# Optimization experiments

Hardware: AMD Instinct MI355X
Metric: run time of the kernel (lower is better)

Reference implementation:

```python
import jax, jax.numpy as jnp
import numpy as np

VOL = (256, 256, 256)
K = 64  # number of connected components (clusters)


def setup_inputs() -> dict:
    key = jax.random.key(0)
    k1, k2, k3 = jax.random.split(key, 3)
    # Precomputed connected-component labels of (pred + target) > 0.
    # 0 = background, 1..K = clusters.
    labels = jax.random.randint(k1, VOL, 0, K + 1, dtype=jnp.int32)
    fg = labels > 0
    # Binary prediction / ground-truth masks, nonzero only inside labeled regions
    # (consistent with labels being components of the overlay of pred and target).
    pred = ((jax.random.uniform(k2, VOL) < 0.6) & fg).astype(jnp.float32)
    target = ((jax.random.uniform(k3, VOL) < 0.6) & fg).astype(jnp.float32)
    return {"pred": pred, "target": target, "labels": labels, "num_clusters": K}


def reference(pred, target, labels, num_clusters):
    # Per-cluster dice via one fused segment reduction instead of a Python loop
    # over clusters. Segment 0 is background and is dropped, matching
    # range(1, num_features + 1) in the original.
    lab = labels.reshape(-1)
    p = pred.reshape(-1)
    t = target.reshape(-1)
    nseg = num_clusters + 1
    # intersection = sum(pred_cluster * gt_cluster); pred/target are binary so
    # logical_and(...).float() products reduce to pred * target per segment.
    inter = jax.ops.segment_sum(p * t, lab, num_segments=nseg)[1:]
    sum_p = jax.ops.segment_sum(p, lab, num_segments=nseg)[1:]
    sum_t = jax.ops.segment_sum(t, lab, num_segments=nseg)[1:]
    union = sum_p + sum_t
    dice = jnp.where(union > 0, 2.0 * inter / jnp.maximum(union, 1.0), 1.0)
    return 1.0 - jnp.mean(dice)
```

## Files before the change

kernel.cpp:

```cpp
#include <hip/hip_runtime.h>


#define NBIN 65
#define NREP 64
#define REP_MASK 63
#define BLOCKS 1024
#define THREADS 256

__device__ __forceinline__ unsigned short contrib16(float p, float t) {
    unsigned int sp = (p != 0.0f) ? 1u : 0u;
    unsigned int st = (t != 0.0f) ? 1u : 0u;
    return (unsigned short)(((sp & st) << 8) | (sp + st));
}

__device__ __forceinline__ void rmw4(unsigned short* col, float4 p, float4 t, int4 l) {
    col[l.x * THREADS] = (unsigned short)(col[l.x * THREADS] + contrib16(p.x, t.x));
    col[l.y * THREADS] = (unsigned short)(col[l.y * THREADS] + contrib16(p.y, t.y));
    col[l.z * THREADS] = (unsigned short)(col[l.z * THREADS] + contrib16(p.z, t.z));
    col[l.w * THREADS] = (unsigned short)(col[l.w * THREADS] + contrib16(p.w, t.w));
}

__global__ __launch_bounds__(THREADS, 4) void seg_count_kernel(
    const float* __restrict__ pred,
    const float* __restrict__ target,
    const int* __restrict__ labels,
    unsigned long long* __restrict__ part,
    int n)
{
    __shared__ unsigned short s_hist[NBIN][THREADS];
    const int tid = threadIdx.x;
    const int rep = (int)blockIdx.x & REP_MASK;

    unsigned int* hz = (unsigned int*)s_hist;
    for (int i = tid; i < NBIN * THREADS / 2; i += THREADS) hz[i] = 0u;
    __syncthreads();

    const int n_vec = n >> 2;
    const float4* __restrict__ p4 = (const float4*)pred;
    const float4* __restrict__ t4 = (const float4*)target;
    const int4*   __restrict__ l4 = (const int4*)labels;

    const int chunk = (n_vec + (int)gridDim.x - 1) / (int)gridDim.x;
    const int base = blockIdx.x * chunk;
    const int end = min(base + chunk, n_vec);

    unsigned short* col = &s_hist[0][tid];

    int idx = base + tid;
    for (; idx + 3 * THREADS < end; idx += 4 * THREADS) {
        float4 p0 = p4[idx];
        float4 p1 = p4[idx + THREADS];
        float4 p2 = p4[idx + 2 * THREADS];
        float4 p3 = p4[idx + 3 * THREADS];
        float4 t0 = t4[idx];
        float4 t1 = t4[idx + THREADS];
        float4 t2 = t4[idx + 2 * THREADS];
        float4 t3 = t4[idx + 3 * THREADS];
        int4   l0 = l4[idx];
        int4   l1 = l4[idx + THREADS];
        int4   l2 = l4[idx + 2 * THREADS];
        int4   l3 = l4[idx + 3 * THREADS];
        __builtin_amdgcn_sched_barrier(0);
        rmw4(col, p0, t0, l0);
        rmw4(col, p1, t1, l1);
        rmw4(col, p2, t2, l2);
        rmw4(col, p3, t3, l3);
    }
    for (; idx < end; idx += THREADS)
        rmw4(col, p4[idx], t4[idx], l4[idx]);

    if (blockIdx.x == 0) {
        for (int i = (n_vec << 2) + tid; i < n; i += THREADS)
            col[labels[i] * THREADS] =
                (unsigned short)(col[labels[i] * THREADS] + contrib16(pred[i], target[i]));
    }
    __syncthreads();

    const int s = 1 + (tid >> 2);
    const int q = tid & 3;
    const unsigned long long* row = (const unsigned long long*)&s_hist[s][q * 64];
    unsigned long long accU = 0, accI = 0;
    const int rot = tid & 15;
    #pragma unroll
    for (int j = 0; j < 16; ++j) {
        int i = (j + rot) & 15;
        unsigned long long v = row[i];
        accU += v & 0x00FF00FF00FF00FFull;
        accI += (v >> 8) & 0x00FF00FF00FF00FFull;
    }
    accU += accU >> 32;
    accI += accI >> 32;
    unsigned int U = ((unsigned int)accU & 0xFFFFu) + (((unsigned int)accU >> 16) & 0xFFFFu);
    unsigned int I = ((unsigned int)accI & 0xFFFFu) + (((unsigned int)accI >> 16) & 0xFFFFu);

    U += __shfl_xor(U, 1); U += __shfl_xor(U, 2);
    I += __shfl_xor(I, 1); I += __shfl_xor(I, 2);
    if (q == 0) {
        unsigned long long tot = ((unsigned long long)I << 32) | (unsigned long long)U;
        if (tot) atomicAdd(&part[(s - 1) * NREP + rep], tot);
    }
}

__global__ __launch_bounds__(256) void dice_finalize_kernel(
    const unsigned long long* __restrict__ part,
    const int* __restrict__ nc_ptr,
    float* __restrict__ out)
{
    const int nc = *nc_ptr;
    const int tid = threadIdx.x;
    const int s = 1 + (tid >> 2);
    const int q = tid & 3;

    unsigned long long acc = 0;
    const unsigned long long* row = part + (s - 1) * NREP + q * 16;
    #pragma unroll
    for (int i = 0; i < 16; ++i) acc += row[i];
    acc += __shfl_xor(acc, 1);
    acc += __shfl_xor(acc, 2);

    __shared__ float s_dice[64];
    if (q == 0) {
        float U = (float)(unsigned int)(acc & 0xFFFFFFFFull);
        float I = (float)(unsigned int)(acc >> 32);
        float dice = (U > 0.0f) ? (2.0f * I / U) : 1.0f;
        s_dice[s - 1] = (s <= nc) ? dice : 0.0f;
    }
    __syncthreads();

    if (tid < 64) {
        float local = s_dice[tid];
        #pragma unroll
        for (int off = 32; off > 0; off >>= 1)
            local += __shfl_down(local, off);
        if (tid == 0) out[0] = 1.0f - local / (float)nc;
    }
}

extern "C" void kernel_launch(void* const* d_in, const int* in_sizes, int n_in,
                              void* d_out, int out_size, void* d_ws, size_t ws_size,
                              hipStream_t stream) {
    const float* pred   = (const float*)d_in[0];
    const float* target = (const float*)d_in[1];
    const int*   labels = (const int*)d_in[2];
    const int*   nc_ptr = (const int*)d_in[3];
    float* out = (float*)d_out;
    unsigned long long* part = (unsigned long long*)d_ws;

    const int n = in_sizes[0];

    hipMemsetAsync(d_ws, 0, 64 * NREP * sizeof(unsigned long long), stream);

    seg_count_kernel<<<BLOCKS, THREADS, 0, stream>>>(
        pred, target, labels, part, n);
    dice_finalize_kernel<<<1, 256, 0, stream>>>(part, nc_ptr, out);
}
```

Measured before the change: 205.3 us.

## Double-buffer global loads with inline asm and batch LDS histogram updates

Replaces the single-stage unrolled loop with a hand-scheduled two-buffer pipeline that issues dwordx4 loads through inline asm and waits with explicit vmcnt counts, so the next batch of loads is in flight while the current batch updates the histogram. Each group of four elements now reads all four LDS bins before computing contributions and forwards partial sums when labels collide, which removes the serial read-after-write dependence between updates. Launch bounds drop from 4 to 3 waves, allowing more registers for the doubled buffers at the cost of occupancy. The fast path only runs when a block's chunk is exactly 16*THREADS vectors; other sizes fall back to a simple loop.

```diff
diff --git a/kernel.cpp b/kernel.cpp
--- a/kernel.cpp
+++ b/kernel.cpp
@@ -7,20 +7,68 @@
 #define BLOCKS 1024
 #define THREADS 256
 
-__device__ __forceinline__ unsigned short contrib16(float p, float t) {
+typedef float4 f4;
+typedef int4 i4;
+
+#define GLOAD(dst, voff, base) \
+    asm volatile("global_load_dwordx4 %0, %1, %2" \
+                 : "=v"(dst) : "v"(voff), "s"(base))
+
+#define WAITN(NSTR) do { \
+    asm volatile("s_waitcnt vmcnt(" NSTR ")" ::: "memory"); \
+    __builtin_amdgcn_sched_barrier(0); \
+} while (0)
+
+#define ISSUE(X) do { \
+    GLOAD(P##X##0, vo0, pred);   GLOAD(P##X##1, vo1, pred); \
+    GLOAD(P##X##2, vo2, pred);   GLOAD(P##X##3, vo3, pred); \
+    GLOAD(T##X##0, vo0, target); GLOAD(T##X##1, vo1, target); \
+    GLOAD(T##X##2, vo2, target); GLOAD(T##X##3, vo3, target); \
+    GLOAD(L##X##0, vo0, labels); GLOAD(L##X##1, vo1, labels); \
+    GLOAD(L##X##2, vo2, labels); GLOAD(L##X##3, vo3, labels); \
+} while (0)
+
+#define ADV() do { vo0 += 16384u; vo1 += 16384u; vo2 += 16384u; vo3 += 16384u; } while (0)
+
+#define PROCESS(X) do { \
+    rmw_group(hist, tid, P##X##0, T##X##0, L##X##0); \
+    rmw_group(hist, tid, P##X##1, T##X##1, L##X##1); \
+    rmw_group(hist, tid, P##X##2, T##X##2, L##X##2); \
+    rmw_group(hist, tid, P##X##3, T##X##3, L##X##3); \
+} while (0)
+
+__device__ __forceinline__ unsigned int contrib(float p, float t) {
     unsigned int sp = (p != 0.0f) ? 1u : 0u;
     unsigned int st = (t != 0.0f) ? 1u : 0u;
-    return (unsigned short)(((sp & st) << 8) | (sp + st));
-}
-
-__device__ __forceinline__ void rmw4(unsigned short* col, float4 p, float4 t, int4 l) {
-    col[l.x * THREADS] = (unsigned short)(col[l.x * THREADS] + contrib16(p.x, t.x));
-    col[l.y * THREADS] = (unsigned short)(col[l.y * THREADS] + contrib16(p.y, t.y));
-    col[l.z * THREADS] = (unsigned short)(col[l.z * THREADS] + contrib16(p.z, t.z));
-    col[l.w * THREADS] = (unsigned short)(col[l.w * THREADS] + contrib16(p.w, t.w));
-}
-
-__global__ __launch_bounds__(THREADS, 4) void seg_count_kernel(
+    return ((sp & st) << 8) | (sp + st);
+}
+
+__device__ __forceinline__ void rmw_group(unsigned short* hist, int tid,
+                                          f4 p, f4 t, i4 l) {
+    const int i0 = l.x * THREADS + tid;
+    const int i1 = l.y * THREADS + tid;
+    const int i2 = l.z * THREADS + tid;
+    const int i3 = l.w * THREADS + tid;
+    const unsigned int d0 = hist[i0];
+    const unsigned int d1 = hist[i1];
+    const unsigned int d2 = hist[i2];
+    const unsigned int d3 = hist[i3];
+    const unsigned int c0 = contrib(p.x, t.x);
+    const unsigned int c1 = contrib(p.y, t.y);
+    const unsigned int c2 = contrib(p.z, t.z);
+    const unsigned int c3 = contrib(p.w, t.w);
+    const unsigned int e0 = c0;
+    const unsigned int e1 = c1 + ((i1 == i0) ? e0 : 0u);
+    const unsigned int e2 = c2 + ((i2 == i1) ? e1 : ((i2 == i0) ? e0 : 0u));
+    const unsigned int e3 = c3 + ((i3 == i2) ? e2 :
+                             ((i3 == i1) ? e1 : ((i3 == i0) ? e0 : 0u)));
+    hist[i0] = (unsigned short)(d0 + e0);
+    hist[i1] = (unsigned short)(d1 + e1);
+    hist[i2] = (unsigned short)(d2 + e2);
+    hist[i3] = (unsigned short)(d3 + e3);
+}
+
+__global__ __launch_bounds__(THREADS, 3) void seg_count_kernel(
     const float* __restrict__ pred,
     const float* __restrict__ target,
     const int* __restrict__ labels,
@@ -30,55 +78,61 @@
     __shared__ unsigned short s_hist[NBIN][THREADS];
     const int tid = threadIdx.x;
     const int rep = (int)blockIdx.x & REP_MASK;
+    unsigned short* hist = &s_hist[0][0];
 
     unsigned int* hz = (unsigned int*)s_hist;
     for (int i = tid; i < NBIN * THREADS / 2; i += THREADS) hz[i] = 0u;
     __syncthreads();
 
     const int n_vec = n >> 2;
-    const float4* __restrict__ p4 = (const float4*)pred;
-    const float4* __restrict__ t4 = (const float4*)target;
-    const int4*   __restrict__ l4 = (const int4*)labels;
-
     const int chunk = (n_vec + (int)gridDim.x - 1) / (int)gridDim.x;
     const int base = blockIdx.x * chunk;
     const int end = min(base + chunk, n_vec);
 
-    unsigned short* col = &s_hist[0][tid];
-
-    int idx = base + tid;
-    for (; idx + 3 * THREADS < end; idx += 4 * THREADS) {
-        float4 p0 = p4[idx];
-        float4 p1 = p4[idx + THREADS];
-        float4 p2 = p4[idx + 2 * THREADS];
-        float4 p3 = p4[idx + 3 * THREADS];
-        float4 t0 = t4[idx];
-        float4 t1 = t4[idx + THREADS];
-        float4 t2 = t4[idx + 2 * THREADS];
-        float4 t3 = t4[idx + 3 * THREADS];
-        int4   l0 = l4[idx];
-        int4   l1 = l4[idx + THREADS];
-        int4   l2 = l4[idx + 2 * THREADS];
-        int4   l3 = l4[idx + 3 * THREADS];
-        __builtin_amdgcn_sched_barrier(0);
-        rmw4(col, p0, t0, l0);
-        rmw4(col, p1, t1, l1);
-        rmw4(col, p2, t2, l2);
-        rmw4(col, p3, t3, l3);
-    }
-    for (; idx < end; idx += THREADS)
-        rmw4(col, p4[idx], t4[idx], l4[idx]);
+    if (end - base == 16 * THREADS) {
+        f4 PA0, PA1, PA2, PA3, TA0, TA1, TA2, TA3;
+        f4 PB0, PB1, PB2, PB3, TB0, TB1, TB2, TB3;
+        i4 LA0, LA1, LA2, LA3, LB0, LB1, LB2, LB3;
+        unsigned int vo0 = (unsigned int)(base + tid) * 16u;
+        unsigned int vo1 = vo0 + 4096u;
+        unsigned int vo2 = vo0 + 8192u;
+        unsigned int vo3 = vo0 + 12288u;
+
+        ISSUE(A);
+        ADV();
+        ISSUE(B);
+        WAITN("12");
+        PROCESS(A);
+        ADV();
+        ISSUE(A);
+        WAITN("12");
+        PROCESS(B);
+        ADV();
+        ISSUE(B);
+        WAITN("12");
+        PROCESS(A);
+        WAITN("0");
+        PROCESS(B);
+    } else {
+        const f4* __restrict__ p4 = (const f4*)pred;
+        const f4* __restrict__ t4 = (const f4*)target;
+        const i4* __restrict__ l4 = (const i4*)labels;
+        for (int idx = base + tid; idx < end; idx += THREADS)
+            rmw_group(hist, tid, p4[idx], t4[idx], l4[idx]);
+    }
 
     if (blockIdx.x == 0) {
         for (int i = (n_vec << 2) + tid; i < n; i += THREADS)
-            col[labels[i] * THREADS] =
-                (unsigned short)(col[labels[i] * THREADS] + contrib16(pred[i], target[i]));
+            hist[labels[i] * THREADS + tid] =
+                (unsigned short)(hist[labels[i] * THREADS + tid] +
+                                 contrib(pred[i], target[i]));
     }
     __syncthreads();
 
     const int s = 1 + (tid >> 2);
     const int q = tid & 3;
-    const unsigned long long* row = (const unsigned long long*)&s_hist[s][q * 64];
+    const unsigned long long* row =
+        (const unsigned long long*)&s_hist[s][q * 64];
     unsigned long long accU = 0, accI = 0;
     const int rot = tid & 15;
     #pragma unroll
@@ -96,7 +150,8 @@
     U += __shfl_xor(U, 1); U += __shfl_xor(U, 2);
     I += __shfl_xor(I, 1); I += __shfl_xor(I, 2);
     if (q == 0) {
-        unsigned long long tot = ((unsigned long long)I << 32) | (unsigned long long)U;
+        unsigned long long tot =
+            ((unsigned long long)I << 32) | (unsigned long long)U;
         if (tot) atomicAdd(&part[(s - 1) * NREP + rep], tot);
     }
 }
```

Result: no change. 202.9 us (-1.1%).
